# Performance work log

Hardware: AMD Instinct MI355X
Metric: run time of the kernel (lower is better)

Reference implementation:

```python
import jax, jax.numpy as jnp
import numpy as np

HIDDEN_DIM = 64


def setup_inputs() -> dict:
    key = jax.random.key(0)
    k1, k2, k3, k4, k5 = jax.random.split(key, 5)
    B, C, H, W = 4, HIDDEN_DIM, 80, 80
    query = jax.random.normal(k1, (B, C, H, W), dtype=jnp.float32)
    keys = jax.random.normal(k2, (B, C, H, W), dtype=jnp.float32)
    values = jax.random.normal(k3, (B, C, H, W), dtype=jnp.float32)
    # 1x1 conv == per-pixel linear: weight [C_out, C_in], bias [C_out]
    fan_in = C  # kernel_size=1 -> fan_in = C*1*1
    bound = 1.0 / np.sqrt(fan_in)
    Wq = jax.random.uniform(k4, (C, C), dtype=jnp.float32, minval=-bound, maxval=bound)
    bq = jax.random.uniform(k5, (C,), dtype=jnp.float32, minval=-bound, maxval=bound)
    return {"query": query, "keys": keys, "values": values, "Wq": Wq, "bq": bq}


def reference(query, keys, values, Wq, bq):
    B, C, H, W = query.shape
    scale = C ** (-0.5)
    # 1x1 conv projection of query
    qp = jnp.einsum('bchw,dc->bdhw', query, Wq) + bq[None, :, None, None]
    q = qp.reshape(B, C, H * W).transpose(0, 2, 1)       # [B, N, C]
    k = keys.reshape(B, C, H * W)                        # [B, C, N]
    attn = jax.nn.softmax(jnp.einsum('bnc,bcm->bnm', q, k) * scale, axis=-1)  # [B, N, N]
    v = values.reshape(B, C, H * W).transpose(0, 2, 1)   # [B, N, C]
    context = jnp.einsum('bnm,bmc->bnc', attn, v)        # [B, N, C]
    return context.transpose(0, 2, 1).reshape(B, C, H, W)
```

## Files before the change

### kernel.cpp

```cpp
#include <hip/hip_runtime.h>
#include <hip/hip_bf16.h>


#define NPIX 6400
#define SZ 1638400
#define SHIFT2 11.541560327111707f

typedef float f32x4 __attribute__((ext_vector_type(4)));
typedef short bf16x8 __attribute__((ext_vector_type(8)));

#if defined(__has_builtin)
#if __has_builtin(__builtin_amdgcn_sched_barrier)
#define SCHED_FENCE() __builtin_amdgcn_sched_barrier(0)
#endif
#if __has_builtin(__builtin_amdgcn_exp2f)
#define EXP2(x) __builtin_amdgcn_exp2f(x)
#endif
#endif
#ifndef SCHED_FENCE
#define SCHED_FENCE()
#endif
#ifndef EXP2
#define EXP2(x) exp2f(x)
#endif

__device__ __forceinline__ void split2(float x, short& h, short& l) {
  unsigned xb = __float_as_uint(x);
  h = (short)(xb >> 16);
  float r = x - __uint_as_float(xb & 0xffff0000u);
  l = (short)(__float_as_uint(r) >> 16);
}

__device__ __forceinline__ short rne_bf16(float x) {
  unsigned u = __float_as_uint(x);
  return (short)((u + 0x7fffu + ((u >> 16) & 1u)) >> 16);
}

__device__ __forceinline__ unsigned pk2(float a, float b) {
  __hip_bfloat162 t = __float22bfloat162_rn(make_float2(a, b));
  unsigned r;
  __builtin_memcpy(&r, &t, 4);
  return r;
}

__global__ __launch_bounds__(256, 2) void prep(
    const float* __restrict__ query, const float* __restrict__ keys,
    const float* __restrict__ values, const float* __restrict__ Wq,
    const float* __restrict__ bq, short* __restrict__ ws)
{
  const int tid = threadIdx.x;
  const int w = tid >> 6;
  const int lane = tid & 63, l16 = lane & 15, qq = lane >> 4;
  short* Qh = ws;          short* Ql = ws + SZ;
  short* Kh = ws + 2 * SZ; short* Kl = ws + 3 * SZ;
  short* Vh = ws + 4 * SZ;
  const int x = blockIdx.x;

  __shared__ float T[64 * 65];

  if (x < 400) {
    const int b = x / 100, t64 = x % 100;
    const int m0 = t64 * 64;
    const float* kb = keys + (size_t)b * 64 * NPIX;
    {
      const int ch = tid >> 2, ml = (tid & 3) * 4;
      const float* src = kb + (size_t)ch * NPIX + m0 + ml;
      #pragma unroll
      for (int u = 0; u < 4; ++u)
        *(float4*)&T[ch * 65 + ml + 16 * u] = *(const float4*)(src + 16 * u);
    }
    __syncthreads();
    const int mi = t64 * 4 + w;
    #pragma unroll
    for (int c0 = 0; c0 < 2; ++c0) {
      float t[8];
      #pragma unroll
      for (int j = 0; j < 8; ++j)
        t[j] = T[(32 * c0 + 8 * qq + j) * 65 + 16 * w + l16];
      bf16x8 h8, l8;
      #pragma unroll
      for (int j = 0; j < 8; ++j) { short h, l; split2(t[j], h, l); h8[j] = h; l8[j] = l; }
      const int off = ((b * 400 + mi) * 2 + c0) * 512 + lane * 8;
      *(bf16x8*)(Kh + off) = h8;
      *(bf16x8*)(Kl + off) = l8;
    }
  } else if (x < 800) {
    const int y = x - 400;
    const int b = y / 100, t64 = y % 100;
    const int r0 = t64 * 64;
    const float* qb = query + (size_t)b * 64 * NPIX;
    {
      const int ch = tid >> 2, ml = (tid & 3) * 4;
      const float* src = qb + (size_t)ch * NPIX + r0 + ml;
      #pragma unroll
      for (int u = 0; u < 4; ++u)
        *(float4*)&T[ch * 65 + ml + 16 * u] = *(const float4*)(src + 16 * u);
    }
    __syncthreads();
    const int mi = t64 * 4 + w;

    float acc[2][8];
    #pragma unroll
    for (int c0 = 0; c0 < 2; ++c0)
      #pragma unroll
      for (int j = 0; j < 8; ++j) acc[c0][j] = 0.f;

    for (int cin4 = 0; cin4 < 64; cin4 += 4) {
      float xv[4];
      #pragma unroll
      for (int u = 0; u < 4; ++u)
        xv[u] = T[(cin4 + u) * 65 + 16 * w + l16];
      #pragma unroll
      for (int c0 = 0; c0 < 2; ++c0)
        #pragma unroll
        for (int j = 0; j < 8; ++j) {
          const float4 wv = *(const float4*)&Wq[(32 * c0 + 8 * qq + j) * 64 + cin4];
          acc[c0][j] += wv.x * xv[0] + wv.y * xv[1] + wv.z * xv[2] + wv.w * xv[3];
        }
    }
    #pragma unroll
    for (int c0 = 0; c0 < 2; ++c0) {
      bf16x8 h8, l8;
      #pragma unroll
      for (int j = 0; j < 8; ++j) {
        float v = (acc[c0][j] + bq[32 * c0 + 8 * qq + j]) * 0.18033688011112042f;
        short h, l; split2(v, h, l);
        h8[j] = h; l8[j] = l;
      }
      const int off = ((b * 400 + mi) * 2 + c0) * 512 + lane * 8;
      *(bf16x8*)(Qh + off) = h8;
      *(bf16x8*)(Ql + off) = l8;
    }
  } else {
    const int gw = (x - 800) * 4 + w;
    const int b = gw / 200, rest = gw % 200;
    const int i = rest / 2, half = rest % 2;
    const float* vb = values + (size_t)b * 64 * NPIX;
    #pragma unroll
    for (int cc = 0; cc < 2; ++cc) {
      const int ct = 2 * half + cc;
      #pragma unroll
      for (int mh = 0; mh < 2; ++mh) {
        const float* vp = vb + (size_t)(16 * ct + l16) * NPIX + 64 * i + 32 * mh + 8 * qq;
        const float4 a  = *(const float4*)vp;
        const float4 b4 = *(const float4*)(vp + 4);
        const float t[8] = {a.x, a.y, a.z, a.w, b4.x, b4.y, b4.z, b4.w};
        bf16x8 h8;
        #pragma unroll
        for (int j = 0; j < 8; ++j) h8[j] = rne_bf16(t[j]);
        const int off = (((b * 100 + i) * 8) + ct * 2 + mh) * 512 + lane * 8;
        *(bf16x8*)(Vh + off) = h8;
      }
    }
  }
}

__global__ __launch_bounds__(512, 2) void attn_main(
    const short* __restrict__ ws, float* __restrict__ out)
{
  const int tid  = threadIdx.x;
  const int w    = tid >> 6;
  const int lane = tid & 63;
  const int l16  = lane & 15, qq = lane >> 4;
  const int x = blockIdx.x;
  const int b      = x & 3;
  const int rowjob = x >> 2;
  const int rb     = rowjob * 64;

  const short* Qh = ws;
  const short* Kh = ws + 2 * SZ;
  const short* Vh = ws + 4 * SZ;
  float* ob = out + (size_t)b * 64 * NPIX;

  __shared__ char smem[43008];
  short* P   = ((short*)smem) + (w << 11);
  short* QL  = ((short*)smem) + 16384;
  float* OC  = (float*)smem;
  float* LST = (float*)(smem + 40960);

  bf16x8 qfh[4][2];
  {
    const short* qp = Qh + (size_t)((b * 400 + rowjob * 4) * 2) * 512 + lane * 8;
    #pragma unroll
    for (int s = 0; s < 4; ++s)
      #pragma unroll
      for (int c0 = 0; c0 < 2; ++c0) {
        qfh[s][c0] = *(const bf16x8*)(qp + (s * 2 + c0) * 512);
        *(bf16x8*)(QL + ((s * 2 + c0) * 64 + lane) * 8) =
            *(const bf16x8*)(qp + SZ + (s * 2 + c0) * 512);
      }
  }
  __syncthreads();

  f32x4 zero4 = {0.f, 0.f, 0.f, 0.f};
  f32x4 oacc[4][4];
  f32x4 lacc[4];
  #pragma unroll
  for (int ct = 0; ct < 4; ++ct)
    #pragma unroll
    for (int s = 0; s < 4; ++s) oacc[ct][s] = zero4;
  #pragma unroll
  for (int s = 0; s < 4; ++s) lacc[s] = zero4;

  bf16x8 onesA;
  #pragma unroll
  for (int j = 0; j < 8; ++j) onesA[j] = (short)0x3F80;

  bf16x8 kfh[2][2], kfl[2][2];
  bf16x8 vfh[4];

  auto loadK = [&](int i2) {
    const short* kp = Kh + (size_t)((b * 400 + 2 * i2) * 2) * 512 + lane * 8;
    #pragma unroll
    for (int mt = 0; mt < 2; ++mt)
      #pragma unroll
      for (int c0 = 0; c0 < 2; ++c0) {
        kfh[mt][c0] = *(const bf16x8*)(kp + (mt * 2 + c0) * 512);
        kfl[mt][c0] = *(const bf16x8*)(kp + SZ + (mt * 2 + c0) * 512);
      }
  };
  auto loadV = [&](int i2) {
    const short* vp = Vh + (size_t)((b * 100 + (i2 >> 1)) * 8) * 512 + lane * 8;
    #pragma unroll
    for (int ct = 0; ct < 4; ++ct)
      vfh[ct] = *(const bf16x8*)(vp + (ct * 2 + (i2 & 1)) * 512);
  };

  const int i0 = w * 25;
  loadK(i0);
  loadV(i0);

  for (int it = 0; it < 25; ++it) {
    const int i2 = i0 + it;
    const int inext = (it == 24) ? i0 : i2 + 1;

    f32x4 a0[4], a1[4];
    #pragma unroll
    for (int s = 0; s < 4; ++s) {
      f32x4 t0 = zero4, t1 = zero4;
      #pragma unroll
      for (int c0 = 0; c0 < 2; ++c0) {
        const bf16x8 ql = *(const bf16x8*)(QL + ((s * 2 + c0) * 64 + lane) * 8);
        t0 = __builtin_amdgcn_mfma_f32_16x16x32_bf16(kfh[0][c0], qfh[s][c0], t0, 0, 0, 0);
        t0 = __builtin_amdgcn_mfma_f32_16x16x32_bf16(kfh[0][c0], ql,         t0, 0, 0, 0);
        t0 = __builtin_amdgcn_mfma_f32_16x16x32_bf16(kfl[0][c0], qfh[s][c0], t0, 0, 0, 0);
        t1 = __builtin_amdgcn_mfma_f32_16x16x32_bf16(kfh[1][c0], qfh[s][c0], t1, 0, 0, 0);
        t1 = __builtin_amdgcn_mfma_f32_16x16x32_bf16(kfh[1][c0], ql,         t1, 0, 0, 0);
        t1 = __builtin_amdgcn_mfma_f32_16x16x32_bf16(kfl[1][c0], qfh[s][c0], t1, 0, 0, 0);
      }
      a0[s] = t0; a1[s] = t1;
    }

    SCHED_FENCE();
    loadK(inext);
    SCHED_FENCE();

    #pragma unroll
    for (int s = 0; s < 4; ++s) {
      float p0 = EXP2(a0[s][0] - SHIFT2), p1 = EXP2(a0[s][1] - SHIFT2);
      float p2 = EXP2(a0[s][2] - SHIFT2), p3 = EXP2(a0[s][3] - SHIFT2);
      float p4 = EXP2(a1[s][0] - SHIFT2), p5 = EXP2(a1[s][1] - SHIFT2);
      float p6 = EXP2(a1[s][2] - SHIFT2), p7 = EXP2(a1[s][3] - SHIFT2);
      union { unsigned u[2]; short4 s4; } ua, ub;
      ua.u[0] = pk2(p0, p1); ua.u[1] = pk2(p2, p3);
      ub.u[0] = pk2(p4, p5); ub.u[1] = pk2(p6, p7);
      const int gbase = (s * 4 + (qq >> 1)) * 16 + l16;
      *(short4*)(P + (gbase * 8 + 4 * (qq & 1))) = ua.s4;
      *(short4*)(P + ((gbase + 32) * 8 + 4 * (qq & 1))) = ub.s4;
    }

    bf16x8 pf[4];
    #pragma unroll
    for (int s = 0; s < 4; ++s)
      pf[s] = *(const bf16x8*)(P + (((s * 4 + qq) * 16 + l16) * 8));

    #pragma unroll
    for (int ct = 0; ct < 4; ++ct)
      #pragma unroll
      for (int s = 0; s < 4; ++s)
        oacc[ct][s] = __builtin_amdgcn_mfma_f32_16x16x32_bf16(vfh[ct], pf[s], oacc[ct][s], 0, 0, 0);
    #pragma unroll
    for (int s = 0; s < 4; ++s)
      lacc[s] = __builtin_amdgcn_mfma_f32_16x16x32_bf16(onesA, pf[s], lacc[s], 0, 0, 0);

    SCHED_FENCE();
    loadV(inext);
    SCHED_FENCE();
  }

  if (qq == 0) {
    #pragma unroll
    for (int s = 0; s < 4; ++s) LST[w * 64 + s * 16 + l16] = lacc[s][0];
  }
  __syncthreads();

  #pragma unroll
  for (int wp = 0; wp < 8; ++wp) {
    if (w == wp) {
      #pragma unroll
      for (int ct = 0; ct < 4; ++ct)
        #pragma unroll
        for (int s = 0; s < 4; ++s)
          #pragma unroll
          for (int r = 0; r < 4; ++r) {
            const int c = 16 * ct + 4 * qq + r;
            const int idx = c * 65 + 16 * s + l16;
            if (wp == 0) OC[idx] = oacc[ct][s][r];
            else         OC[idx] += oacc[ct][s][r];
          }
    }
    __syncthreads();
  }

  {
    const int r  = tid & 63;
    const int cg = tid >> 6;
    float lsum = 0.f;
    #pragma unroll
    for (int w2 = 0; w2 < 8; ++w2)
      lsum += LST[w2 * 64 + (r >> 4) * 16 + (r & 15)];
    const float inv = 1.0f / lsum;
    #pragma unroll
    for (int u = 0; u < 8; ++u) {
      const int c = cg * 8 + u;
      ob[(size_t)c * NPIX + rb + r] = OC[c * 65 + r] * inv;
    }
  }
}

extern "C" void kernel_launch(void* const* d_in, const int* in_sizes, int n_in,
                              void* d_out, int out_size, void* d_ws, size_t ws_size,
                              hipStream_t stream) {
  const float* query  = (const float*)d_in[0];
  const float* keys   = (const float*)d_in[1];
  const float* values = (const float*)d_in[2];
  const float* Wq     = (const float*)d_in[3];
  const float* bq     = (const float*)d_in[4];
  short* ws = (short*)d_ws;
  prep<<<dim3(1000), dim3(256), 0, stream>>>(query, keys, values, Wq, bq, ws);
  attn_main<<<dim3(400), dim3(512), 0, stream>>>(ws, (float*)d_out);
}
```

Measured before the change: 186.9 us.

## Split warps into QK/softmax producers and PV consumers with double-buffered P

Warps 0-3 now compute QK scores and exp into a double-buffered shared P tile, and warps 4-7 consume the previous tile for the PV and row-sum MFMAs, with a block-wide barrier after every step. Each pair now covers 50 key chunks instead of each warp covering 25. Q-high fragments move from registers into shared memory to cut register pressure, and the explicit scheduling fences are removed. The aim is to overlap the exp work with the PV matrix ops across warps. The cost is 51 block-wide syncs per block, a pipeline fill step, extra LDS reads of Q, and half the warps doing each stage.

Measured after the change: 205.1 us. 1.1x slower.

```diff
diff --git a/kernel.cpp b/kernel.cpp
--- a/kernel.cpp
+++ b/kernel.cpp
@@ -10,15 +10,9 @@
 typedef short bf16x8 __attribute__((ext_vector_type(8)));
 
 #if defined(__has_builtin)
-#if __has_builtin(__builtin_amdgcn_sched_barrier)
-#define SCHED_FENCE() __builtin_amdgcn_sched_barrier(0)
-#endif
 #if __has_builtin(__builtin_amdgcn_exp2f)
 #define EXP2(x) __builtin_amdgcn_exp2f(x)
 #endif
-#endif
-#ifndef SCHED_FENCE
-#define SCHED_FENCE()
 #endif
 #ifndef EXP2
 #define EXP2(x) exp2f(x)
@@ -172,25 +166,30 @@
   const short* Vh = ws + 4 * SZ;
   float* ob = out + (size_t)b * 64 * NPIX;
 
-  __shared__ char smem[43008];
-  short* P   = ((short*)smem) + (w << 11);
-  short* QL  = ((short*)smem) + 16384;
+  __shared__ char smem[50176];
+  short* PB  = (short*)smem;
+  short* QH  = ((short*)smem) + 16384;
+  short* QL  = ((short*)smem) + 20480;
+  float* LST = (float*)(smem + 49152);
   float* OC  = (float*)smem;
-  float* LST = (float*)(smem + 40960);
-
-  bf16x8 qfh[4][2];
+
   {
     const short* qp = Qh + (size_t)((b * 400 + rowjob * 4) * 2) * 512 + lane * 8;
     #pragma unroll
     for (int s = 0; s < 4; ++s)
       #pragma unroll
       for (int c0 = 0; c0 < 2; ++c0) {
-        qfh[s][c0] = *(const bf16x8*)(qp + (s * 2 + c0) * 512);
+        *(bf16x8*)(QH + ((s * 2 + c0) * 64 + lane) * 8) =
+            *(const bf16x8*)(qp + (s * 2 + c0) * 512);
         *(bf16x8*)(QL + ((s * 2 + c0) * 64 + lane) * 8) =
             *(const bf16x8*)(qp + SZ + (s * 2 + c0) * 512);
       }
   }
   __syncthreads();
+
+  const int  p     = w & 3;
+  const bool isP   = (w < 4);
+  const int  cbase = p * 50;
 
   f32x4 zero4 = {0.f, 0.f, 0.f, 0.f};
   f32x4 oacc[4][4];
@@ -226,77 +225,75 @@
       vfh[ct] = *(const bf16x8*)(vp + (ct * 2 + (i2 & 1)) * 512);
   };
 
-  const int i0 = w * 25;
-  loadK(i0);
-  loadV(i0);
-
-  for (int it = 0; it < 25; ++it) {
-    const int i2 = i0 + it;
-    const int inext = (it == 24) ? i0 : i2 + 1;
-
-    f32x4 a0[4], a1[4];
-    #pragma unroll
-    for (int s = 0; s < 4; ++s) {
-      f32x4 t0 = zero4, t1 = zero4;
-      #pragma unroll
-      for (int c0 = 0; c0 < 2; ++c0) {
-        const bf16x8 ql = *(const bf16x8*)(QL + ((s * 2 + c0) * 64 + lane) * 8);
-        t0 = __builtin_amdgcn_mfma_f32_16x16x32_bf16(kfh[0][c0], qfh[s][c0], t0, 0, 0, 0);
-        t0 = __builtin_amdgcn_mfma_f32_16x16x32_bf16(kfh[0][c0], ql,         t0, 0, 0, 0);
-        t0 = __builtin_amdgcn_mfma_f32_16x16x32_bf16(kfl[0][c0], qfh[s][c0], t0, 0, 0, 0);
-        t1 = __builtin_amdgcn_mfma_f32_16x16x32_bf16(kfh[1][c0], qfh[s][c0], t1, 0, 0, 0);
-        t1 = __builtin_amdgcn_mfma_f32_16x16x32_bf16(kfh[1][c0], ql,         t1, 0, 0, 0);
-        t1 = __builtin_amdgcn_mfma_f32_16x16x32_bf16(kfl[1][c0], qfh[s][c0], t1, 0, 0, 0);
-      }
-      a0[s] = t0; a1[s] = t1;
-    }
-
-    SCHED_FENCE();
-    loadK(inext);
-    SCHED_FENCE();
-
-    #pragma unroll
-    for (int s = 0; s < 4; ++s) {
-      float p0 = EXP2(a0[s][0] - SHIFT2), p1 = EXP2(a0[s][1] - SHIFT2);
-      float p2 = EXP2(a0[s][2] - SHIFT2), p3 = EXP2(a0[s][3] - SHIFT2);
-      float p4 = EXP2(a1[s][0] - SHIFT2), p5 = EXP2(a1[s][1] - SHIFT2);
-      float p6 = EXP2(a1[s][2] - SHIFT2), p7 = EXP2(a1[s][3] - SHIFT2);
-      union { unsigned u[2]; short4 s4; } ua, ub;
-      ua.u[0] = pk2(p0, p1); ua.u[1] = pk2(p2, p3);
-      ub.u[0] = pk2(p4, p5); ub.u[1] = pk2(p6, p7);
-      const int gbase = (s * 4 + (qq >> 1)) * 16 + l16;
-      *(short4*)(P + (gbase * 8 + 4 * (qq & 1))) = ua.s4;
-      *(short4*)(P + ((gbase + 32) * 8 + 4 * (qq & 1))) = ub.s4;
-    }
-
-    bf16x8 pf[4];
-    #pragma unroll
-    for (int s = 0; s < 4; ++s)
-      pf[s] = *(const bf16x8*)(P + (((s * 4 + qq) * 16 + l16) * 8));
-
-    #pragma unroll
-    for (int ct = 0; ct < 4; ++ct)
-      #pragma unroll
-      for (int s = 0; s < 4; ++s)
-        oacc[ct][s] = __builtin_amdgcn_mfma_f32_16x16x32_bf16(vfh[ct], pf[s], oacc[ct][s], 0, 0, 0);
-    #pragma unroll
-    for (int s = 0; s < 4; ++s)
-      lacc[s] = __builtin_amdgcn_mfma_f32_16x16x32_bf16(onesA, pf[s], lacc[s], 0, 0, 0);
-
-    SCHED_FENCE();
-    loadV(inext);
-    SCHED_FENCE();
-  }
-
-  if (qq == 0) {
-    #pragma unroll
-    for (int s = 0; s < 4; ++s) LST[w * 64 + s * 16 + l16] = lacc[s][0];
-  }
-  __syncthreads();
+  if (isP) loadK(cbase);
+  else     loadV(cbase);
+
+  for (int t = 0; t <= 50; ++t) {
+    if (isP) {
+      if (t < 50) {
+        const int c = cbase + t;
+        short* PW = PB + ((p * 2 + (t & 1)) << 11);
+        f32x4 a0[4], a1[4];
+        #pragma unroll
+        for (int s = 0; s < 4; ++s) {
+          f32x4 t0 = zero4, t1 = zero4;
+          #pragma unroll
+          for (int c0 = 0; c0 < 2; ++c0) {
+            const bf16x8 qh = *(const bf16x8*)(QH + ((s * 2 + c0) * 64 + lane) * 8);
+            const bf16x8 ql = *(const bf16x8*)(QL + ((s * 2 + c0) * 64 + lane) * 8);
+            t0 = __builtin_amdgcn_mfma_f32_16x16x32_bf16(kfh[0][c0], qh, t0, 0, 0, 0);
+            t0 = __builtin_amdgcn_mfma_f32_16x16x32_bf16(kfh[0][c0], ql, t0, 0, 0, 0);
+            t0 = __builtin_amdgcn_mfma_f32_16x16x32_bf16(kfl[0][c0], qh, t0, 0, 0, 0);
+            t1 = __builtin_amdgcn_mfma_f32_16x16x32_bf16(kfh[1][c0], qh, t1, 0, 0, 0);
+            t1 = __builtin_amdgcn_mfma_f32_16x16x32_bf16(kfh[1][c0], ql, t1, 0, 0, 0);
+            t1 = __builtin_amdgcn_mfma_f32_16x16x32_bf16(kfl[1][c0], qh, t1, 0, 0, 0);
+          }
+          a0[s] = t0; a1[s] = t1;
+        }
+        loadK(t < 49 ? c + 1 : cbase);
+        #pragma unroll
+        for (int s = 0; s < 4; ++s) {
+          float p0 = EXP2(a0[s][0] - SHIFT2), p1 = EXP2(a0[s][1] - SHIFT2);
+          float p2 = EXP2(a0[s][2] - SHIFT2), p3 = EXP2(a0[s][3] - SHIFT2);
+          float p4 = EXP2(a1[s][0] - SHIFT2), p5 = EXP2(a1[s][1] - SHIFT2);
+          float p6 = EXP2(a1[s][2] - SHIFT2), p7 = EXP2(a1[s][3] - SHIFT2);
+          union { unsigned u[2]; short4 s4; } ua, ub;
+          ua.u[0] = pk2(p0, p1); ua.u[1] = pk2(p2, p3);
+          ub.u[0] = pk2(p4, p5); ub.u[1] = pk2(p6, p7);
+          const int gbase = (s * 4 + (qq >> 1)) * 16 + l16;
+          *(short4*)(PW + (gbase * 8 + 4 * (qq & 1))) = ua.s4;
+          *(short4*)(PW + ((gbase + 32) * 8 + 4 * (qq & 1))) = ub.s4;
+        }
+      }
+    } else {
+      if (t >= 1) {
+        const short* PR = PB + ((p * 2 + ((t - 1) & 1)) << 11);
+        bf16x8 pf[4];
+        #pragma unroll
+        for (int s = 0; s < 4; ++s)
+          pf[s] = *(const bf16x8*)(PR + (((s * 4 + qq) * 16 + l16) * 8));
+        #pragma unroll
+        for (int ct = 0; ct < 4; ++ct)
+          #pragma unroll
+          for (int s = 0; s < 4; ++s)
+            oacc[ct][s] = __builtin_amdgcn_mfma_f32_16x16x32_bf16(vfh[ct], pf[s], oacc[ct][s], 0, 0, 0);
+        #pragma unroll
+        for (int s = 0; s < 4; ++s)
+          lacc[s] = __builtin_amdgcn_mfma_f32_16x16x32_bf16(onesA, pf[s], lacc[s], 0, 0, 0);
+        loadV(t < 50 ? cbase + t : cbase);
+      }
+    }
+    __syncthreads();
+  }
+
+  if (!isP && qq == 0) {
+    #pragma unroll
+    for (int s = 0; s < 4; ++s) LST[p * 64 + s * 16 + l16] = lacc[s][0];
+  }
 
   #pragma unroll
-  for (int wp = 0; wp < 8; ++wp) {
-    if (w == wp) {
+  for (int wp = 0; wp < 4; ++wp) {
+    if (w == 4 + wp) {
       #pragma unroll
       for (int ct = 0; ct < 4; ++ct)
         #pragma unroll
@@ -317,7 +314,7 @@
     const int cg = tid >> 6;
     float lsum = 0.f;
     #pragma unroll
-    for (int w2 = 0; w2 < 8; ++w2)
+    for (int w2 = 0; w2 < 4; ++w2)
       lsum += LST[w2 * 64 + (r >> 4) * 16 + (r & 15)];
     const float inv = 1.0f / lsum;
     #pragma unroll
```
